# Kernel tuning notes

Measured on AMD Instinct MI355X. Metric: run time of the kernel, lower is better.

## Reference

```python
import jax, jax.numpy as jnp
import numpy as np

N2, N1, N0 = 16000, 4000, 1000   # leaf / mid / target node counts
DEG = 32                          # sampled neighbors per target
IN_DIM, OUT_DIM, H = 256, 64, 4
NEG = -9e15
ALPHA = 0.2                       # LeakyReLU slope


def setup_inputs() -> dict:
    key = jax.random.key(0)
    ks = jax.random.split(key, 10)
    s = 0.05  # xavier-ish scale
    x = jax.random.normal(ks[0], (N2, IN_DIM), jnp.float32)
    W0 = jax.random.normal(ks[1], (H, IN_DIM, OUT_DIM), jnp.float32) * s
    a0 = jax.random.normal(ks[2], (H, 2 * OUT_DIM), jnp.float32) * s
    W1 = jax.random.normal(ks[3], (H, OUT_DIM * H, OUT_DIM), jnp.float32) * s
    a1 = jax.random.normal(ks[4], (H, 2 * OUT_DIM), jnp.float32) * s
    lin_W = jax.random.normal(ks[5], (OUT_DIM * H, OUT_DIM * H), jnp.float32) * s
    lin_b = jax.random.normal(ks[6], (OUT_DIM * H,), jnp.float32) * s
    # level-1 edges: n1 targets, each with DEG sampled leaf neighbors + self-loop
    adj1_tgt = jnp.concatenate([jnp.repeat(jnp.arange(N1), DEG), jnp.arange(N1)]).astype(jnp.int32)
    adj1_nbr = jnp.concatenate([jax.random.randint(ks[7], (N1 * DEG,), 0, N2),
                                jnp.arange(N1)]).astype(jnp.int32)
    # level-0 edges: n0 targets, each with DEG sampled mid neighbors + self-loop
    adj0_tgt = jnp.concatenate([jnp.repeat(jnp.arange(N0), DEG), jnp.arange(N0)]).astype(jnp.int32)
    adj0_nbr = jnp.concatenate([jax.random.randint(ks[8], (N0 * DEG,), 0, N1),
                                jnp.arange(N0)]).astype(jnp.int32)
    return {"x": x, "W0": W0, "a0": a0, "W1": W1, "a1": a1,
            "lin_W": lin_W, "lin_b": lin_b,
            "adj1_tgt": adj1_tgt, "adj1_nbr": adj1_nbr,
            "adj0_tgt": adj0_tgt, "adj0_nbr": adj0_nbr,
            "n0": N0, "n1": N1}


def _att_layer(x, W, a, tgt, nbr, T):
    # x: [N, D], W: [H, D, O], a: [H, 2O]; multi-head GAT layer (eval mode, no dropout)
    h = jnp.einsum('nd,hdo->hno', x, W)                      # [H, N, O]
    O = h.shape[-1]
    e = jax.nn.leaky_relu(
        jnp.einsum('heo,ho->he', h[:, tgt], a[:, :O]) +
        jnp.einsum('heo,ho->he', h[:, nbr], a[:, O:]), ALPHA)  # [H, E]
    N = h.shape[1]
    att = jnp.full((h.shape[0], T, N), NEG, x.dtype).at[:, tgt, nbr].set(e)
    att = jax.nn.softmax(att, axis=-1)                        # dense edge-softmax
    hp = jax.nn.elu(jnp.einsum('htn,hno->hto', att, h))       # [H, T, O]
    return jnp.transpose(hp, (1, 0, 2)).reshape(T, -1)        # cat heads -> [T, H*O]


def reference(x, W0, a0, W1, a1, lin_W, lin_b,
              adj1_tgt, adj1_nbr, adj0_tgt, adj0_nbr, n0, n1):
    x1 = _att_layer(x, W0, a0, adj1_tgt, adj1_nbr, n1)   # [n1, H*O]
    x2 = _att_layer(x1, W1, a1, adj0_tgt, adj0_nbr, n0)  # [n0, H*O]
    return jnp.tanh(x2 @ lin_W.T + lin_b)                # Linear + Tanh
```

## Files before the change

### kernel.cpp

```cpp
#include <hip/hip_runtime.h>
#include <math.h>

#define N2C 16000
#define N1C 4000
#define N0C 1000
#define DEG 32
#define NHEAD 4
#define ALPHA 0.2f
#define LDP 264

typedef __attribute__((ext_vector_type(8))) short bf16x8;
typedef __attribute__((ext_vector_type(4))) float f32x4;

__device__ __forceinline__ ushort f2bf(float f) {
    unsigned u = __float_as_uint(f);
    unsigned r = (u + 0x7fffu + ((u >> 16) & 1u)) >> 16;
    return (ushort)r;
}
__device__ __forceinline__ float bf2f(ushort h) {
    return __uint_as_float(((unsigned)h) << 16);
}
__device__ __forceinline__ unsigned long long pack4(ushort a, ushort b, ushort c, ushort d) {
    return (unsigned long long)a | ((unsigned long long)b << 16) |
           ((unsigned long long)c << 32) | ((unsigned long long)d << 48);
}

__global__ __launch_bounds__(256) void repack_kernel(
    const float* __restrict__ W0, const float* __restrict__ W1,
    const float* __restrict__ linW,
    ushort* __restrict__ Wth, ushort* __restrict__ Wtl, float* __restrict__ linWT)
{
    const int b = blockIdx.x;
    if (b >= 512) {
        int idx = (b - 512) * 256 + threadIdx.x;
        int k = idx >> 8, c = idx & 255;
        __builtin_nontemporal_store(linW[c * 256 + k], &linWT[k * 256 + c]);
        return;
    }
    int g = b * 256 + threadIdx.x;
    int mat = g >> 16;
    int idx = g & 65535;
    int c = idx >> 8, k = idx & 255;
    const float* W = mat ? W1 : W0;
    float v = W[(c >> 6) * (256 * 64) + k * 64 + (c & 63)];
    ushort h = f2bf(v);
    __builtin_nontemporal_store(h, &Wth[g]);
    __builtin_nontemporal_store(f2bf(v - bf2f(h)), &Wtl[g]);
}

__global__ __launch_bounds__(256) void gemm1_kernel(
    const float* __restrict__ Af,
    const ushort* __restrict__ Bh, const ushort* __restrict__ Bl,
    const float* __restrict__ avec,
    float* __restrict__ out, float* __restrict__ s_t, float* __restrict__ s_n)
{
    __shared__ ushort sah[32 * LDP];
    __shared__ ushort sal[32 * LDP];
    const int wave = threadIdx.x >> 6, lane = threadIdx.x & 63;
    const int quad = lane >> 4, l16 = lane & 15;
    const int row0 = blockIdx.x * 32;
    const int col0 = wave * 64;

    for (int idx = threadIdx.x; idx < 32 * 64; idx += 256) {
        int row = idx >> 6, c4 = idx & 63;
        float4 f = ((const float4*)Af)[(size_t)(row0 + row) * 64 + c4];
        ushort4 h, l;
        h.x = f2bf(f.x); l.x = f2bf(f.x - bf2f(h.x));
        h.y = f2bf(f.y); l.y = f2bf(f.y - bf2f(h.y));
        h.z = f2bf(f.z); l.z = f2bf(f.z - bf2f(h.z));
        h.w = f2bf(f.w); l.w = f2bf(f.w - bf2f(h.w));
        *(ushort4*)(&sah[row * LDP + c4 * 4]) = h;
        *(ushort4*)(&sal[row * LDP + c4 * 4]) = l;
    }
    __syncthreads();

    f32x4 acc[2][4];
#pragma unroll
    for (int r = 0; r < 2; ++r)
#pragma unroll
        for (int c = 0; c < 4; ++c) acc[r][c] = (f32x4){0.f, 0.f, 0.f, 0.f};
    const int kbase = quad * 8;

    for (int k0 = 0; k0 < 256; k0 += 32) {
        bf16x8 a_h[2], a_l[2], b_h[4], b_l[4];
#pragma unroll
        for (int r = 0; r < 2; ++r) {
            int loff = (r * 16 + l16) * LDP + k0 + kbase;
            a_h[r] = *(const bf16x8*)(&sah[loff]);
            a_l[r] = *(const bf16x8*)(&sal[loff]);
        }
#pragma unroll
        for (int c = 0; c < 4; ++c) {
            int off = (col0 + c * 16 + l16) * 256 + k0 + kbase;
            b_h[c] = *(const bf16x8*)(Bh + off);
            b_l[c] = *(const bf16x8*)(Bl + off);
        }
#pragma unroll
        for (int r = 0; r < 2; ++r)
#pragma unroll
            for (int c = 0; c < 4; ++c) {
                acc[r][c] = __builtin_amdgcn_mfma_f32_16x16x32_bf16(a_h[r], b_h[c], acc[r][c], 0, 0, 0);
                acc[r][c] = __builtin_amdgcn_mfma_f32_16x16x32_bf16(a_h[r], b_l[c], acc[r][c], 0, 0, 0);
                acc[r][c] = __builtin_amdgcn_mfma_f32_16x16x32_bf16(a_l[r], b_h[c], acc[r][c], 0, 0, 0);
            }
    }

#pragma unroll
    for (int r = 0; r < 2; ++r)
#pragma unroll
        for (int c = 0; c < 4; ++c) {
            int col = col0 + c * 16 + l16;
#pragma unroll
            for (int reg = 0; reg < 4; ++reg) {
                int row = row0 + r * 16 + quad * 4 + reg;
                __builtin_nontemporal_store(acc[r][c][reg], &out[(size_t)row * 256 + col]);
            }
        }

    float at[4], an[4];
#pragma unroll
    for (int c = 0; c < 4; ++c) {
        at[c] = avec[wave * 128 + c * 16 + l16];
        an[c] = avec[wave * 128 + 64 + c * 16 + l16];
    }
#pragma unroll
    for (int r = 0; r < 2; ++r) {
        float pt[4] = {0.f, 0.f, 0.f, 0.f}, pn[4] = {0.f, 0.f, 0.f, 0.f};
#pragma unroll
        for (int c = 0; c < 4; ++c)
#pragma unroll
            for (int reg = 0; reg < 4; ++reg) {
                pt[reg] += acc[r][c][reg] * at[c];
                pn[reg] += acc[r][c][reg] * an[c];
            }
#pragma unroll
        for (int reg = 0; reg < 4; ++reg)
#pragma unroll
            for (int m = 1; m < 16; m <<= 1) {
                pt[reg] += __shfl_xor(pt[reg], m);
                pn[reg] += __shfl_xor(pn[reg], m);
            }
        if (l16 == 0) {
#pragma unroll
            for (int reg = 0; reg < 4; ++reg) {
                int row = row0 + r * 16 + quad * 4 + reg;
                __builtin_nontemporal_store(pt[reg], &s_t[wave * N2C + row]);
                __builtin_nontemporal_store(pn[reg], &s_n[wave * N2C + row]);
            }
        }
    }
}

__global__ __launch_bounds__(256) void att_kernel(
    const float* __restrict__ hprev, const int* __restrict__ nbr_arr,
    const float* __restrict__ s_t, const float* __restrict__ s_n,
    ushort* __restrict__ outhi, ushort* __restrict__ outlo, int T, int Nsrc)
{
    __shared__ int nbr[DEG + 1];
    __shared__ float att_s[NHEAD][DEG + 3];
    __shared__ float4 red[4][64];
    const int tgt = blockIdx.x;
    const int t = threadIdx.x;
    const int lane = t & 63;
    if (t < DEG) nbr[t] = nbr_arr[tgt * DEG + t];
    else if (t == DEG) nbr[DEG] = nbr_arr[T * DEG + tgt];
    __syncthreads();

    {
        const int hd = t >> 6;
        int me = (lane <= DEG) ? nbr[lane] : -1;
        int k = (lane <= DEG) ? 1 : 0;
#pragma unroll
        for (int j = 0; j < DEG; ++j) {
            int v = __shfl(me, j);
            if (j < lane && v == me) k = 0;
        }
        float e = s_t[hd * Nsrc + tgt] + ((lane <= DEG) ? s_n[hd * Nsrc + me] : 0.f);
        e = (e >= 0.f) ? e : ALPHA * e;
        float em = k ? e : -1e30f;
        float m = em;
#pragma unroll
        for (int off = 1; off < 64; off <<= 1) m = fmaxf(m, __shfl_xor(m, off));
        float w = k ? __expf(e - m) : 0.f;
        float Z = w;
#pragma unroll
        for (int off = 1; off < 64; off <<= 1) Z += __shfl_xor(Z, off);
        if (lane <= DEG) att_s[hd][lane] = w / Z;
    }
    __syncthreads();

    const int cq = t & 63;
    const int rg = t >> 6;
    const int hd = cq >> 4;
    const float4* hp4 = (const float4*)hprev;
    float4 acc = make_float4(0.f, 0.f, 0.f, 0.f);
#pragma unroll
    for (int ii = 0; ii < 9; ++ii) {
        int i = rg + ii * 4;
        if (i <= DEG) {
            float w = att_s[hd][i];
            float4 v = hp4[(size_t)nbr[i] * 64 + cq];
            acc.x += w * v.x; acc.y += w * v.y;
            acc.z += w * v.z; acc.w += w * v.w;
        }
    }
    red[rg][cq] = acc;
    __syncthreads();
    if (t < 64) {
        float4 s0 = red[0][t], s1 = red[1][t], s2 = red[2][t], s3 = red[3][t];
        float4 s;
        s.x = s0.x + s1.x + s2.x + s3.x;
        s.y = s0.y + s1.y + s2.y + s3.y;
        s.z = s0.z + s1.z + s2.z + s3.z;
        s.w = s0.w + s1.w + s2.w + s3.w;
        s.x = (s.x > 0.f) ? s.x : expm1f(s.x);
        s.y = (s.y > 0.f) ? s.y : expm1f(s.y);
        s.z = (s.z > 0.f) ? s.z : expm1f(s.z);
        s.w = (s.w > 0.f) ? s.w : expm1f(s.w);
        ushort hx = f2bf(s.x), hy = f2bf(s.y), hz = f2bf(s.z), hw = f2bf(s.w);
        ushort lx = f2bf(s.x - bf2f(hx)), ly = f2bf(s.y - bf2f(hy));
        ushort lz = f2bf(s.z - bf2f(hz)), lw = f2bf(s.w - bf2f(hw));
        __builtin_nontemporal_store(pack4(hx, hy, hz, hw),
            &((unsigned long long*)outhi)[tgt * 64 + t]);
        __builtin_nontemporal_store(pack4(lx, ly, lz, lw),
            &((unsigned long long*)outlo)[tgt * 64 + t]);
    }
}

__global__ __launch_bounds__(256) void gemm2_kernel(
    const ushort* __restrict__ Ah, const ushort* __restrict__ Al,
    const ushort* __restrict__ Bh, const ushort* __restrict__ Bl,
    const float* __restrict__ avec,
    float* __restrict__ h1, float* __restrict__ st2, float* __restrict__ sn2)
{
    const int wave = threadIdx.x >> 6, lane = threadIdx.x & 63;
    const int quad = lane >> 4, l16 = lane & 15;
    const int row0 = blockIdx.x * 16;
    const int col0 = wave * 64;
    const int kbase = quad * 8;
    const int arow = row0 + l16;

    f32x4 acc2[4];
#pragma unroll
    for (int c = 0; c < 4; ++c) acc2[c] = (f32x4){0.f, 0.f, 0.f, 0.f};

    for (int k0 = 0; k0 < 256; k0 += 32) {
        bf16x8 a_h, a_l, b_h[4], b_l[4];
        int aoff = arow * 256 + k0 + kbase;
        a_h = *(const bf16x8*)(Ah + aoff);
        a_l = *(const bf16x8*)(Al + aoff);
#pragma unroll
        for (int c = 0; c < 4; ++c) {
            int off = (col0 + c * 16 + l16) * 256 + k0 + kbase;
            b_h[c] = *(const bf16x8*)(Bh + off);
            b_l[c] = *(const bf16x8*)(Bl + off);
        }
#pragma unroll
        for (int c = 0; c < 4; ++c) {
            acc2[c] = __builtin_amdgcn_mfma_f32_16x16x32_bf16(a_h, b_h[c], acc2[c], 0, 0, 0);
            acc2[c] = __builtin_amdgcn_mfma_f32_16x16x32_bf16(a_h, b_l[c], acc2[c], 0, 0, 0);
            acc2[c] = __builtin_amdgcn_mfma_f32_16x16x32_bf16(a_l, b_h[c], acc2[c], 0, 0, 0);
        }
    }
#pragma unroll
    for (int c = 0; c < 4; ++c) {
        int col = col0 + c * 16 + l16;
#pragma unroll
        for (int reg = 0; reg < 4; ++reg) {
            int row = row0 + quad * 4 + reg;
            __builtin_nontemporal_store(acc2[c][reg], &h1[(size_t)row * 256 + col]);
        }
    }

    float at[4], an[4];
#pragma unroll
    for (int c = 0; c < 4; ++c) {
        at[c] = avec[wave * 128 + c * 16 + l16];
        an[c] = avec[wave * 128 + 64 + c * 16 + l16];
    }
    float pt[4] = {0.f, 0.f, 0.f, 0.f}, pn[4] = {0.f, 0.f, 0.f, 0.f};
#pragma unroll
    for (int c = 0; c < 4; ++c)
#pragma unroll
        for (int reg = 0; reg < 4; ++reg) {
            pt[reg] += acc2[c][reg] * at[c];
            pn[reg] += acc2[c][reg] * an[c];
        }
#pragma unroll
    for (int reg = 0; reg < 4; ++reg)
#pragma unroll
        for (int m = 1; m < 16; m <<= 1) {
            pt[reg] += __shfl_xor(pt[reg], m);
            pn[reg] += __shfl_xor(pn[reg], m);
        }
    if (l16 == 0) {
#pragma unroll
        for (int reg = 0; reg < 4; ++reg) {
            int row = row0 + quad * 4 + reg;
            __builtin_nontemporal_store(pt[reg], &st2[wave * N1C + row]);
            __builtin_nontemporal_store(pn[reg], &sn2[wave * N1C + row]);
        }
    }
}

__global__ __launch_bounds__(256) void att_lin_kernel(
    const float* __restrict__ h1, const int* __restrict__ nbr_arr,
    const float* __restrict__ s_t, const float* __restrict__ s_n,
    const float* __restrict__ linWT, const float* __restrict__ bias,
    float* __restrict__ out)
{
    __shared__ int   nbr_s[4][DEG + 1];
    __shared__ float att_w[4][NHEAD][DEG + 1];
    __shared__ float x2[4][256];

    const int wave = threadIdx.x >> 6, lane = threadIdx.x & 63;
    const int blk = blockIdx.x;

    for (int idx = threadIdx.x; idx < 4 * (DEG + 1); idx += 256) {
        int tt = idx / (DEG + 1), e = idx - tt * (DEG + 1);
        nbr_s[tt][e] = (e < DEG) ? nbr_arr[(blk * 4 + tt) * DEG + e]
                                 : nbr_arr[N0C * DEG + blk * 4 + tt];
    }
    __syncthreads();

    {
        const int tl = wave;
        const int gt = blk * 4 + tl;
        int me = (lane <= DEG) ? nbr_s[tl][lane] : 0;
        int k = (lane <= DEG) ? 1 : 0;
#pragma unroll
        for (int j = 0; j < DEG; ++j) {
            int v = __shfl(me, j);
            if (j < lane && v == me) k = 0;
        }
#pragma unroll
        for (int hd = 0; hd < NHEAD; ++hd) {
            float e = s_t[hd * N1C + gt] + s_n[hd * N1C + me];
            e = (e >= 0.f) ? e : ALPHA * e;
            float em = k ? e : -1e30f;
            float m = em;
#pragma unroll
            for (int off = 1; off < 64; off <<= 1) m = fmaxf(m, __shfl_xor(m, off));
            float w = k ? __expf(e - m) : 0.f;
            float Z = w;
#pragma unroll
            for (int off = 1; off < 64; off <<= 1) Z += __shfl_xor(Z, off);
            if (lane <= DEG) att_w[tl][hd][lane] = w / Z;
        }
    }
    __syncthreads();
    {
        const int tl = wave;
        const int hh = lane >> 4;
        float4 acc = make_float4(0.f, 0.f, 0.f, 0.f);
#pragma unroll
        for (int e = 0; e <= DEG; ++e) {
            float w = att_w[tl][hh][e];
            float4 v = ((const float4*)h1)[(size_t)nbr_s[tl][e] * 64 + lane];
            acc.x += w * v.x; acc.y += w * v.y;
            acc.z += w * v.z; acc.w += w * v.w;
        }
        acc.x = (acc.x > 0.f) ? acc.x : expm1f(acc.x);
        acc.y = (acc.y > 0.f) ? acc.y : expm1f(acc.y);
        acc.z = (acc.z > 0.f) ? acc.z : expm1f(acc.z);
        acc.w = (acc.w > 0.f) ? acc.w : expm1f(acc.w);
        *(float4*)(&x2[tl][lane * 4]) = acc;
    }
    __syncthreads();

    const int c = threadIdx.x;
    float v0 = 0.f, v1 = 0.f, v2 = 0.f, v3 = 0.f;
#pragma unroll 8
    for (int k = 0; k < 256; ++k) {
        float wv = linWT[k * 256 + c];
        v0 += x2[0][k] * wv;
        v1 += x2[1][k] * wv;
        v2 += x2[2][k] * wv;
        v3 += x2[3][k] * wv;
    }
    float b = bias[c];
    out[(size_t)(blk * 4 + 0) * 256 + c] = tanhf(v0 + b);
    out[(size_t)(blk * 4 + 1) * 256 + c] = tanhf(v1 + b);
    out[(size_t)(blk * 4 + 2) * 256 + c] = tanhf(v2 + b);
    out[(size_t)(blk * 4 + 3) * 256 + c] = tanhf(v3 + b);
}

extern "C" void kernel_launch(void* const* d_in, const int* in_sizes, int n_in,
                              void* d_out, int out_size, void* d_ws, size_t ws_size,
                              hipStream_t stream)
{
    const float* x    = (const float*)d_in[0];
    const float* W0   = (const float*)d_in[1];
    const float* a0   = (const float*)d_in[2];
    const float* W1   = (const float*)d_in[3];
    const float* a1   = (const float*)d_in[4];
    const float* linW = (const float*)d_in[5];
    const float* linb = (const float*)d_in[6];
    const int* adj1_nbr = (const int*)d_in[8];
    const int* adj0_nbr = (const int*)d_in[10];

    char* base = (char*)d_ws;
    ushort* Wth = (ushort*)base;
    ushort* Wtl = (ushort*)(base + 262144);
    float*  linWT = (float*)(base + 524288);
    float*  st  = (float*)(base + 786432);
    float*  sn  = (float*)(base + 1048576);
    float*  st2 = (float*)(base + 1310720);
    float*  sn2 = (float*)(base + 1376256);
    ushort* xhi = (ushort*)(base + 1441792);
    ushort* xlo = (ushort*)(base + 3538944);
    float*  h0  = (float*)(base + 5636096);
    float*  h1  = (float*)(base + 22020096);

    repack_kernel<<<768, 256, 0, stream>>>(W0, W1, linW, Wth, Wtl, linWT);

    gemm1_kernel<<<N2C / 32, 256, 0, stream>>>(x, Wth, Wtl, a0, h0, st, sn);

    att_kernel<<<N1C, 256, 0, stream>>>(h0, adj1_nbr, st, sn, xhi, xlo, N1C, N2C);

    gemm2_kernel<<<N1C / 16, 256, 0, stream>>>(
        xhi, xlo, Wth + 65536, Wtl + 65536, a1, h1, st2, sn2);

    att_lin_kernel<<<N0C / 4, 256, 0, stream>>>(
        h1, adj0_nbr, st2, sn2, linWT, linb, (float*)d_out);
}
```

Before: 166.7 us.

## Store layer-1 projections in bf16 and fold W1/linW repack into attention kernel

gemm1 now writes the projected features h0 as bf16 instead of fp32, which halves the 16 MB intermediate write and the gathered reads in att_kernel. The W1 and linW repacking moves out of the first repack launch into extra blocks of att_kernel, shrinking the kernel on the critical path before gemm1. The cost is lower precision in the aggregated features, since h0 drops from fp32 to single bf16, which may fail tolerance. The attention logits still use the fp32 scores.

```diff
diff --git a/kernel.cpp b/kernel.cpp
--- a/kernel.cpp
+++ b/kernel.cpp
@@ -26,23 +26,12 @@
 }
 
 __global__ __launch_bounds__(256) void repack_kernel(
-    const float* __restrict__ W0, const float* __restrict__ W1,
-    const float* __restrict__ linW,
-    ushort* __restrict__ Wth, ushort* __restrict__ Wtl, float* __restrict__ linWT)
-{
-    const int b = blockIdx.x;
-    if (b >= 512) {
-        int idx = (b - 512) * 256 + threadIdx.x;
-        int k = idx >> 8, c = idx & 255;
-        __builtin_nontemporal_store(linW[c * 256 + k], &linWT[k * 256 + c]);
-        return;
-    }
-    int g = b * 256 + threadIdx.x;
-    int mat = g >> 16;
-    int idx = g & 65535;
-    int c = idx >> 8, k = idx & 255;
-    const float* W = mat ? W1 : W0;
-    float v = W[(c >> 6) * (256 * 64) + k * 64 + (c & 63)];
+    const float* __restrict__ W0,
+    ushort* __restrict__ Wth, ushort* __restrict__ Wtl)
+{
+    int g = blockIdx.x * 256 + threadIdx.x;
+    int c = g >> 8, k = g & 255;
+    float v = W0[(c >> 6) * (256 * 64) + k * 64 + (c & 63)];
     ushort h = f2bf(v);
     __builtin_nontemporal_store(h, &Wth[g]);
     __builtin_nontemporal_store(f2bf(v - bf2f(h)), &Wtl[g]);
@@ -52,7 +41,7 @@
     const float* __restrict__ Af,
     const ushort* __restrict__ Bh, const ushort* __restrict__ Bl,
     const float* __restrict__ avec,
-    float* __restrict__ out, float* __restrict__ s_t, float* __restrict__ s_n)
+    ushort* __restrict__ outb, float* __restrict__ s_t, float* __restrict__ s_n)
 {
     __shared__ ushort sah[32 * LDP];
     __shared__ ushort sal[32 * LDP];
@@ -113,7 +102,8 @@
 #pragma unroll
             for (int reg = 0; reg < 4; ++reg) {
                 int row = row0 + r * 16 + quad * 4 + reg;
-                __builtin_nontemporal_store(acc[r][c][reg], &out[(size_t)row * 256 + col]);
+                __builtin_nontemporal_store(f2bf(acc[r][c][reg]),
+                                            &outb[(size_t)row * 256 + col]);
             }
         }
 
@@ -152,18 +142,37 @@
 }
 
 __global__ __launch_bounds__(256) void att_kernel(
-    const float* __restrict__ hprev, const int* __restrict__ nbr_arr,
+    const ushort* __restrict__ h0b, const int* __restrict__ nbr_arr,
     const float* __restrict__ s_t, const float* __restrict__ s_n,
-    ushort* __restrict__ outhi, ushort* __restrict__ outlo, int T, int Nsrc)
-{
+    const float* __restrict__ W1, const float* __restrict__ linW,
+    ushort* __restrict__ Wth, ushort* __restrict__ Wtl, float* __restrict__ linWT,
+    ushort* __restrict__ outhi, ushort* __restrict__ outlo)
+{
+    const int b = blockIdx.x;
+    if (b >= N1C) {
+        if (b < N1C + 256) {
+            int idx = (b - N1C) * 256 + threadIdx.x;
+            int c = idx >> 8, k = idx & 255;
+            float v = W1[(c >> 6) * (256 * 64) + k * 64 + (c & 63)];
+            ushort h = f2bf(v);
+            __builtin_nontemporal_store(h, &Wth[65536 + idx]);
+            __builtin_nontemporal_store(f2bf(v - bf2f(h)), &Wtl[65536 + idx]);
+        } else {
+            int idx = (b - N1C - 256) * 256 + threadIdx.x;
+            int k = idx >> 8, c = idx & 255;
+            __builtin_nontemporal_store(linW[c * 256 + k], &linWT[k * 256 + c]);
+        }
+        return;
+    }
+
     __shared__ int nbr[DEG + 1];
     __shared__ float att_s[NHEAD][DEG + 3];
     __shared__ float4 red[4][64];
-    const int tgt = blockIdx.x;
+    const int tgt = b;
     const int t = threadIdx.x;
     const int lane = t & 63;
     if (t < DEG) nbr[t] = nbr_arr[tgt * DEG + t];
-    else if (t == DEG) nbr[DEG] = nbr_arr[T * DEG + tgt];
+    else if (t == DEG) nbr[DEG] = nbr_arr[N1C * DEG + tgt];
     __syncthreads();
 
     {
@@ -175,7 +184,7 @@
             int v = __shfl(me, j);
             if (j < lane && v == me) k = 0;
         }
-        float e = s_t[hd * Nsrc + tgt] + ((lane <= DEG) ? s_n[hd * Nsrc + me] : 0.f);
+        float e = s_t[hd * N2C + tgt] + ((lane <= DEG) ? s_n[hd * N2C + me] : 0.f);
         e = (e >= 0.f) ? e : ALPHA * e;
         float em = k ? e : -1e30f;
         float m = em;
@@ -192,16 +201,18 @@
     const int cq = t & 63;
     const int rg = t >> 6;
     const int hd = cq >> 4;
-    const float4* hp4 = (const float4*)hprev;
+    const unsigned long long* hp8 = (const unsigned long long*)h0b;
     float4 acc = make_float4(0.f, 0.f, 0.f, 0.f);
 #pragma unroll
     for (int ii = 0; ii < 9; ++ii) {
         int i = rg + ii * 4;
         if (i <= DEG) {
             float w = att_s[hd][i];
-            float4 v = hp4[(size_t)nbr[i] * 64 + cq];
-            acc.x += w * v.x; acc.y += w * v.y;
-            acc.z += w * v.z; acc.w += w * v.w;
+            unsigned long long p = hp8[(size_t)nbr[i] * 64 + cq];
+            acc.x += w * bf2f((ushort)p);
+            acc.y += w * bf2f((ushort)(p >> 16));
+            acc.z += w * bf2f((ushort)(p >> 32));
+            acc.w += w * bf2f((ushort)(p >> 48));
         }
     }
     red[rg][cq] = acc;
@@ -409,14 +420,15 @@
     float*  sn2 = (float*)(base + 1376256);
     ushort* xhi = (ushort*)(base + 1441792);
     ushort* xlo = (ushort*)(base + 3538944);
-    float*  h0  = (float*)(base + 5636096);
-    float*  h1  = (float*)(base + 22020096);
-
-    repack_kernel<<<768, 256, 0, stream>>>(W0, W1, linW, Wth, Wtl, linWT);
-
-    gemm1_kernel<<<N2C / 32, 256, 0, stream>>>(x, Wth, Wtl, a0, h0, st, sn);
-
-    att_kernel<<<N1C, 256, 0, stream>>>(h0, adj1_nbr, st, sn, xhi, xlo, N1C, N2C);
+    ushort* h0b = (ushort*)(base + 5636096);
+    float*  h1  = (float*)(base + 13824512);
+
+    repack_kernel<<<256, 256, 0, stream>>>(W0, Wth, Wtl);
+
+    gemm1_kernel<<<N2C / 32, 256, 0, stream>>>(x, Wth, Wtl, a0, h0b, st, sn);
+
+    att_kernel<<<N1C + 512, 256, 0, stream>>>(
+        h0b, adj1_nbr, st, sn, W1, linW, Wth, Wtl, linWT, xhi, xlo);
 
     gemm2_kernel<<<N1C / 16, 256, 0, stream>>>(
         xhi, xlo, Wth + 65536, Wtl + 65536, a1, h1, st2, sn2);
```

Result: faster. 161.6 us (-3.0%).
